# Kernel tuning notes

Hardware: AMD Instinct MI355X
Metric: run time of the kernel (lower is better)

Reference implementation:

```python
import jax, jax.numpy as jnp
import numpy as np

D_MODEL = 256
NHEAD = 8
HEAD_DIM = D_MODEL // NHEAD
LN_EPS = 1e-5


def _layernorm(x, g, b):
    mu = jnp.mean(x, axis=-1, keepdims=True)
    var = jnp.mean(jnp.square(x - mu), axis=-1, keepdims=True)
    return (x - mu) * jax.lax.rsqrt(var + LN_EPS) * g + b


def setup_inputs() -> dict:
    key = jax.random.key(0)
    ks = jax.random.split(key, 12)
    N, L, S, K = 2, 4800, 4800, 64
    x = jax.random.normal(ks[0], (N, L, D_MODEL), dtype=jnp.float32)
    source = jax.random.normal(ks[1], (N, S, D_MODEL), dtype=jnp.float32)
    # precomputed epipolar-band key indices per query ([N, L, K])
    epipolar_idx = jax.random.randint(ks[2], (N, L, K), 0, S, dtype=jnp.int32)
    w = lambda k, shape: (jax.random.normal(k, shape, dtype=jnp.float32) * 0.02)
    return {
        "x": x, "source": source, "epipolar_idx": epipolar_idx,
        "Wq": w(ks[3], (D_MODEL, D_MODEL)),
        "Wk": w(ks[4], (D_MODEL, D_MODEL)),
        "Wv": w(ks[5], (D_MODEL, D_MODEL)),
        "Wm": w(ks[6], (D_MODEL, D_MODEL)),
        "W1": w(ks[7], (2 * D_MODEL, 2 * D_MODEL)),
        "W2": w(ks[8], (2 * D_MODEL, D_MODEL)),
        "g1": jnp.ones((D_MODEL,), jnp.float32),
        "b1": jnp.zeros((D_MODEL,), jnp.float32),
        "g2": jnp.ones((D_MODEL,), jnp.float32),
        "b2": jnp.zeros((D_MODEL,), jnp.float32),
    }


def reference(x, source, epipolar_idx, Wq, Wk, Wv, Wm, W1, W2, g1, b1, g2, b2):
    N, L, _ = x.shape
    q = (x @ Wq).reshape(N, L, NHEAD, HEAD_DIM)            # [N,L,H,D]
    k = (source @ Wk).reshape(N, -1, NHEAD, HEAD_DIM)      # [N,S,H,D]
    v = (source @ Wv).reshape(N, -1, NHEAD, HEAD_DIM)
    # one-to-many gather: each query attends only to its epipolar-band keys
    gather = jax.vmap(lambda t, i: t[i])                   # [N,L,K,H,D]
    kg = gather(k, epipolar_idx)
    vg = gather(v, epipolar_idx)
    scale = 1.0 / jnp.sqrt(jnp.asarray(HEAD_DIM, x.dtype))
    scores = jnp.einsum('nlhd,nlkhd->nlhk', q, kg) * scale
    attn = jax.nn.softmax(scores, axis=-1)
    msg = jnp.einsum('nlhk,nlkhd->nlhd', attn, vg).reshape(N, L, D_MODEL)
    msg = _layernorm(msg @ Wm, g1, b1)
    h = jnp.concatenate([x, msg], axis=-1) @ W1            # [N,L,2C]
    h = jax.nn.relu(h) @ W2                                # [N,L,C]
    return x + _layernorm(h, g2, b2)
```

## Files before the change

kernel.cpp:

```cpp
#include <hip/hip_runtime.h>
#include <hip/hip_bf16.h>

#define D_MODEL 256
#define LQ 4800
#define NB 2
#define MROWS (NB * LQ)
#define LN_EPS 1e-5f

typedef unsigned int u32;
typedef unsigned short u16;
typedef __attribute__((ext_vector_type(8))) short bf16x8;
typedef __attribute__((ext_vector_type(4))) float f32x4;
typedef __attribute__((ext_vector_type(2))) _Float16 f16x2;

__device__ __forceinline__ u16 f2bf(float f) {
    __hip_bfloat16 h = __float2bfloat16(f);
    return *reinterpret_cast<u16*>(&h);
}

__device__ __forceinline__ float dot2f16(u32 a, u32 b, float c) {
#if __has_builtin(__builtin_amdgcn_fdot2)
    return __builtin_amdgcn_fdot2(__builtin_bit_cast(f16x2, a),
                                  __builtin_bit_cast(f16x2, b), c, false);
#else
    f16x2 av = __builtin_bit_cast(f16x2, a), bv = __builtin_bit_cast(f16x2, b);
    c = fmaf((float)av.x, (float)bv.x, c);
    return fmaf((float)av.y, (float)bv.y, c);
#endif
}
__device__ __forceinline__ u32 pk_fma16(u32 a, u32 b, u32 c) {
    u32 d;
    asm("v_pk_fma_f16 %0, %1, %2, %3" : "=v"(d) : "v"(a), "v"(b), "v"(c));
    return d;
}
__device__ __forceinline__ u32 pk_add16(u32 a, u32 b) {
    u32 d;
    asm("v_pk_add_f16 %0, %1, %2" : "=v"(d) : "v"(a), "v"(b));
    return d;
}
__device__ __forceinline__ u32 pkrtz(float a, float b) {
    return __builtin_bit_cast(u32, __builtin_amdgcn_cvt_pkrtz(a, b));
}
__device__ __forceinline__ void gload_lds(const u16* src, u16* dst) {
    __builtin_amdgcn_global_load_lds(
        (const __attribute__((address_space(1))) u32*)src,
        (__attribute__((address_space(3))) u32*)dst, 16, 0, 0);
}

__global__ __launch_bounds__(256) void prep_kernel(
    const float* __restrict__ x, const float* __restrict__ source,
    const float* __restrict__ Wq, const float* __restrict__ Wk,
    const float* __restrict__ Wv, const float* __restrict__ Wm,
    const float* __restrict__ W1, const float* __restrict__ W2,
    u16* __restrict__ xb, u16* __restrict__ sb,
    u16* __restrict__ Wqkvt, u16* __restrict__ Wmt,
    u16* __restrict__ W1t, u16* __restrict__ W2t)
{
    __shared__ float tile[16][17];
    const int t = threadIdx.x;
    int bid = blockIdx.x;

    if (bid < 4800) {
        const float* src = bid < 2400 ? x : source;
        u16* dst = bid < 2400 ? xb : sb;
        int b = bid < 2400 ? bid : bid - 2400;
        int i = (b * 256 + t) * 4;
        float4 v = *reinterpret_cast<const float4*>(src + i);
        ushort4 o; o.x = f2bf(v.x); o.y = f2bf(v.y); o.z = f2bf(v.z); o.w = f2bf(v.w);
        *reinterpret_cast<ushort4*>(dst + i) = o;
        return;
    }
    int sub = bid - 4800;
    const float* W; u16* Wt; int Nd, ldt, rowoff;
    if      (sub < 256)  { W = Wq; Wt = Wqkvt; Nd = 256; ldt = 256; rowoff = 0;   }
    else if (sub < 512)  { W = Wk; Wt = Wqkvt; Nd = 256; ldt = 256; rowoff = 256; sub -= 256; }
    else if (sub < 768)  { W = Wv; Wt = Wqkvt; Nd = 256; ldt = 256; rowoff = 512; sub -= 512; }
    else if (sub < 1024) { W = Wm; Wt = Wmt;   Nd = 256; ldt = 256; rowoff = 0;   sub -= 768; }
    else if (sub < 2048) { W = W1; Wt = W1t;   Nd = 512; ldt = 512; rowoff = 0;   sub -= 1024; }
    else                 { W = W2; Wt = W2t;   Nd = 256; ldt = 512; rowoff = 0;   sub -= 2048; }
    int ntiles = Nd >> 4;
    int tn = sub % ntiles, tk = sub / ntiles;
    int tx = t & 15, ty = t >> 4;
    tile[ty][tx] = W[(size_t)(tk * 16 + ty) * Nd + tn * 16 + tx];
    __syncthreads();
    Wt[(size_t)(rowoff + tn * 16 + ty) * ldt + tk * 16 + tx] = f2bf(tile[tx][ty]);
}

template<int BM, int BN>
__global__ __launch_bounds__(256) void gemm_mfma_kernel(
    const u16* __restrict__ A0, int lda0,
    const u16* __restrict__ A1, int lda1, int splitK, int nsel,
    const u16* __restrict__ Bt, int ldb,
    void* __restrict__ Cout,
    int M, int N, int K, int flags)
{
    __shared__ __align__(16) u16 As[BM * 32];
    __shared__ __align__(16) u16 Bs[BN * 32];

    constexpr int WM = BM / 2, WN = BN / 2;
    constexpr int FI = WM / 16, FJ = WN / 16;

    const int t  = threadIdx.x;
    const int l  = t & 63;
    const int w  = t >> 6;
    const int m0 = blockIdx.y * BM;
    const int n0 = blockIdx.x * BN;
    const int wr = w >> 1, wc = w & 1;

    if (nsel && n0 >= nsel) { A0 = A1; lda0 = lda1; }

    const int srow = l >> 2;
    const int sch  = (l & 3) ^ (srow & 3);

    f32x4 acc[FI][FJ];
#pragma unroll
    for (int i = 0; i < FI; ++i)
#pragma unroll
        for (int j = 0; j < FJ; ++j) acc[i][j] = (f32x4){0.f, 0.f, 0.f, 0.f};

    for (int k0 = 0; k0 < K; k0 += 32) {
        const u16* Ap; int kk, lda;
        if (splitK && k0 >= splitK) { Ap = A1; kk = k0 - splitK; lda = lda1; }
        else                        { Ap = A0; kk = k0;          lda = lda0; }

        if (BM >= 64) {
#pragma unroll
            for (int g = 0; g < BM / 64; ++g) {
                int grp = w * (BM / 64) + g;
                int row = grp * 16 + srow;
                gload_lds(Ap + (size_t)(m0 + row) * lda + kk + sch * 8, As + grp * 512);
            }
        } else if (w < BM / 16) {
            int row = w * 16 + srow;
            gload_lds(Ap + (size_t)(m0 + row) * lda + kk + sch * 8, As + w * 512);
        }
#pragma unroll
        for (int g = 0; g < BN / 64; ++g) {
            int grp = w * (BN / 64) + g;
            int row = grp * 16 + srow;
            gload_lds(Bt + (size_t)(n0 + row) * ldb + k0 + sch * 8, Bs + grp * 512);
        }
        __syncthreads();

        const int r  = l & 15;
        const int ch = l >> 4;
        bf16x8 af[FI], bfr[FJ];
#pragma unroll
        for (int i = 0; i < FI; ++i) {
            int ar = wr * WM + i * 16 + r;
            af[i] = *(const bf16x8*)((const char*)As + ar * 64 + ((ch ^ (r & 3)) * 16));
        }
#pragma unroll
        for (int j = 0; j < FJ; ++j) {
            int br = wc * WN + j * 16 + r;
            bfr[j] = *(const bf16x8*)((const char*)Bs + br * 64 + ((ch ^ (r & 3)) * 16));
        }
#pragma unroll
        for (int i = 0; i < FI; ++i)
#pragma unroll
            for (int j = 0; j < FJ; ++j)
                acc[i][j] = __builtin_amdgcn_mfma_f32_16x16x32_bf16(af[i], bfr[j], acc[i][j], 0, 0, 0);
        __syncthreads();
    }

    const int r  = l & 15;
    const int q4 = l >> 4;
#pragma unroll
    for (int i = 0; i < FI; ++i)
#pragma unroll
        for (int j = 0; j < FJ; ++j) {
            int col = n0 + wc * WN + j * 16 + r;
#pragma unroll
            for (int reg = 0; reg < 4; ++reg) {
                int row = m0 + wr * WM + i * 16 + q4 * 4 + reg;
                float vv = acc[i][j][reg];
                if (flags & 1) vv = fmaxf(vv, 0.f);
                size_t off;
                int colw, Nw;
                if (flags & 4) { off = (size_t)(col >> 8) * M * 256; colw = col & 255; Nw = 256; }
                else           { off = 0; colw = col; Nw = N; }
                if (flags & 8) {
                    _Float16 hv = (_Float16)vv;
                    ((u16*)Cout)[off + (size_t)row * Nw + colw] = __builtin_bit_cast(u16, hv);
                } else if (flags & 2) {
                    ((u16*)Cout)[off + (size_t)row * Nw + colw] = f2bf(vv);
                } else {
                    ((float*)Cout)[off + (size_t)row * Nw + colw] = vv;
                }
            }
        }
}

template<int BM, bool RESID, bool OUT_BF16>
__global__ __launch_bounds__(256) void gemm_ln_kernel(
    const u16* __restrict__ A, int lda,
    const u16* __restrict__ Bt, int ldb,
    const float* __restrict__ g, const float* __restrict__ b,
    const float* __restrict__ xres,
    void* __restrict__ Cout, int K)
{
    constexpr int WAVES_M = BM / 16;
    constexpr int WAVES_N = 4 / WAVES_M;
    constexpr int WN = 256 / WAVES_N;
    constexpr int FJ = WN / 16;

    __shared__ __align__(16) u16 As[BM * 32];
    __shared__ __align__(16) u16 Bs[256 * 32];
    __shared__ float2 red[BM][WAVES_N];

    const int t  = threadIdx.x;
    const int l  = t & 63;
    const int w  = t >> 6;
    const int m0 = blockIdx.x * BM;
    const int wr = w / WAVES_N, wc = w % WAVES_N;

    const int srow = l >> 2;
    const int sch  = (l & 3) ^ (srow & 3);

    f32x4 acc[FJ];
#pragma unroll
    for (int j = 0; j < FJ; ++j) acc[j] = (f32x4){0.f, 0.f, 0.f, 0.f};

    for (int k0 = 0; k0 < K; k0 += 32) {
        if (w < WAVES_M) {
            int row = w * 16 + srow;
            gload_lds(A + (size_t)(m0 + row) * lda + k0 + sch * 8, As + w * 512);
        }
#pragma unroll
        for (int gg = 0; gg < 4; ++gg) {
            int grp = w * 4 + gg;
            int row = grp * 16 + srow;
            gload_lds(Bt + (size_t)row * ldb + k0 + sch * 8, Bs + grp * 512);
        }
        __syncthreads();

        const int r  = l & 15;
        const int ch = l >> 4;
        bf16x8 af = *(const bf16x8*)((const char*)As + (wr * 16 + r) * 64 + ((ch ^ (r & 3)) * 16));
#pragma unroll
        for (int j = 0; j < FJ; ++j) {
            int br = wc * WN + j * 16 + r;
            bf16x8 bf = *(const bf16x8*)((const char*)Bs + br * 64 + ((ch ^ (r & 3)) * 16));
            acc[j] = __builtin_amdgcn_mfma_f32_16x16x32_bf16(af, bf, acc[j], 0, 0, 0);
        }
        __syncthreads();
    }

    const int r  = l & 15;
    const int q4 = l >> 4;

    float rs[4], rq[4];
#pragma unroll
    for (int reg = 0; reg < 4; ++reg) {
        float s = 0.f, sq = 0.f;
#pragma unroll
        for (int j = 0; j < FJ; ++j) { float vv = acc[j][reg]; s += vv; sq += vv * vv; }
        rs[reg] = s; rq[reg] = sq;
    }
#pragma unroll
    for (int off = 1; off <= 8; off <<= 1)
#pragma unroll
        for (int reg = 0; reg < 4; ++reg) {
            rs[reg] += __shfl_xor(rs[reg], off);
            rq[reg] += __shfl_xor(rq[reg], off);
        }
    if (r == 0)
#pragma unroll
        for (int reg = 0; reg < 4; ++reg)
            red[wr * 16 + q4 * 4 + reg][wc] = make_float2(rs[reg], rq[reg]);
    __syncthreads();

    float gj[FJ], bj[FJ];
#pragma unroll
    for (int j = 0; j < FJ; ++j) {
        int col = wc * WN + j * 16 + r;
        gj[j] = g[col]; bj[j] = b[col];
    }

#pragma unroll
    for (int reg = 0; reg < 4; ++reg) {
        int row = wr * 16 + q4 * 4 + reg;
        float sum = 0.f, sq = 0.f;
#pragma unroll
        for (int u = 0; u < WAVES_N; ++u) { sum += red[row][u].x; sq += red[row][u].y; }
        float mu  = sum * 0.00390625f;
        float var = sq * 0.00390625f - mu * mu;
        float rstd = rsqrtf(var + LN_EPS);
#pragma unroll
        for (int j = 0; j < FJ; ++j) {
            int col = wc * WN + j * 16 + r;
            float vv = (acc[j][reg] - mu) * rstd * gj[j] + bj[j];
            size_t oidx = (size_t)(m0 + row) * 256 + col;
            if (RESID) vv += xres[oidx];
            if (OUT_BF16) ((u16*)Cout)[oidx] = f2bf(vv);
            else          ((float*)Cout)[oidx] = vv;
        }
    }
}

__global__ __launch_bounds__(256, 8) void attn_kernel(
    const u16* __restrict__ q, const u16* __restrict__ k,
    const u16* __restrict__ v, const int* __restrict__ idx,
    u16* __restrict__ msg)
{
    const int t  = threadIdx.x;
    const int l  = t & 63;
    const int hp = t >> 6;
    const int qi = blockIdx.x;
    const int n  = qi / LQ;
    const size_t srcbase = (size_t)n * LQ * 256;

    const int o = l >> 3;
    const int c = l & 7;

    const int* idxp = idx + (size_t)qi * 64;
    int rows[8];
#pragma unroll
    for (int i = 0; i < 8; ++i) rows[i] = idxp[i * 8 + o];

    const size_t hoff = (size_t)hp * 64 + c * 8;

    uint4 kd[8];
#pragma unroll
    for (int i = 0; i < 8; ++i)
        kd[i] = *(const uint4*)(k + srcbase + (size_t)rows[i] * 256 + hoff);
    uint4 qc = *(const uint4*)(q + (size_t)qi * 256 + hoff);

    float s[8];
#pragma unroll
    for (int i = 0; i < 8; ++i) {
        float si = 0.f;
        si = dot2f16(kd[i].x, qc.x, si);
        si = dot2f16(kd[i].y, qc.y, si);
        si = dot2f16(kd[i].z, qc.z, si);
        si = dot2f16(kd[i].w, qc.w, si);
        si += __shfl_xor(si, 1);
        si += __shfl_xor(si, 2);
        s[i] = si * 0.17677669529663687f;
    }

    uint4 vd[8];
#pragma unroll
    for (int i = 0; i < 8; ++i)
        vd[i] = *(const uint4*)(v + srcbase + (size_t)rows[i] * 256 + hoff);

    float mx = s[0];
#pragma unroll
    for (int i = 1; i < 8; ++i) mx = fmaxf(mx, s[i]);
    mx = fmaxf(mx, __shfl_xor(mx, 8));
    mx = fmaxf(mx, __shfl_xor(mx, 16));
    mx = fmaxf(mx, __shfl_xor(mx, 32));
    float p[8], sum = 0.f;
#pragma unroll
    for (int i = 0; i < 8; ++i) { p[i] = __expf(s[i] - mx); sum += p[i]; }
    sum += __shfl_xor(sum, 8);
    sum += __shfl_xor(sum, 16);
    sum += __shfl_xor(sum, 32);
    float inv = 1.f / sum;

    u32 A0 = 0, A1 = 0, A2 = 0, A3 = 0;
#pragma unroll
    for (int i = 0; i < 8; ++i) {
        float pi = p[i] * inv;
        u32 pp = pkrtz(pi, pi);
        A0 = pk_fma16(pp, vd[i].x, A0);
        A1 = pk_fma16(pp, vd[i].y, A1);
        A2 = pk_fma16(pp, vd[i].z, A2);
        A3 = pk_fma16(pp, vd[i].w, A3);
    }

    const bool ob0 = (o & 1) != 0;
    const bool ob1 = (o & 2) != 0;
    {
        u32 t0 = ob0 ? A0 : A2;
        u32 t1 = ob0 ? A1 : A3;
        t0 = __shfl_xor((int)t0, 8);
        t1 = __shfl_xor((int)t1, 8);
        A0 = pk_add16(ob0 ? A2 : A0, t0);
        A1 = pk_add16(ob0 ? A3 : A1, t1);
    }
    {
        u32 u0 = ob1 ? A0 : A1;
        u0 = __shfl_xor((int)u0, 16);
        A0 = pk_add16(ob1 ? A1 : A0, u0);
    }
    A0 = pk_add16(A0, (u32)__shfl_xor((int)A0, 32));

    if (o < 4) {
        int j = 2 * (o & 1) + ((o >> 1) & 1);
        f16x2 hv = __builtin_bit_cast(f16x2, A0);
        u32 packed = (u32)f2bf((float)hv.x) | ((u32)f2bf((float)hv.y) << 16);
        *(u32*)(msg + (size_t)qi * 256 + hp * 64 + c * 8 + j * 2) = packed;
    }
}

extern "C" void kernel_launch(void* const* d_in, const int* in_sizes, int n_in,
                              void* d_out, int out_size, void* d_ws, size_t ws_size,
                              hipStream_t stream)
{
    const float* x      = (const float*)d_in[0];
    const float* source = (const float*)d_in[1];
    const int*   eidx   = (const int*)d_in[2];
    const float* Wq     = (const float*)d_in[3];
    const float* Wk     = (const float*)d_in[4];
    const float* Wv     = (const float*)d_in[5];
    const float* Wm     = (const float*)d_in[6];
    const float* W1     = (const float*)d_in[7];
    const float* W2     = (const float*)d_in[8];
    const float* g1     = (const float*)d_in[9];
    const float* b1     = (const float*)d_in[10];
    const float* g2     = (const float*)d_in[11];
    const float* b2     = (const float*)d_in[12];
    float* out = (float*)d_out;

    char* ws = (char*)d_ws;
    const size_t SZB = (size_t)MROWS * 256 * 2;
    u16* xb     = (u16*)(ws);
    u16* sb     = (u16*)(ws + SZB);
    u16* qb     = (u16*)(ws + 2 * SZB);
    u16* kb     = (u16*)(ws + 3 * SZB);
    u16* vb     = (u16*)(ws + 4 * SZB);
    u16* msgb   = (u16*)(ws + 5 * SZB);
    u16* msglnb = (u16*)(ws + 6 * SZB);
    u16* h1b    = (u16*)(ws + 7 * SZB);
    u16* Wqkvt  = (u16*)(ws + 9 * SZB);
    u16* Wmt    = Wqkvt + 768 * 256;
    u16* W1t    = Wmt + 256 * 256;
    u16* W2t    = W1t + 512 * 512;

    dim3 blk(256);

    prep_kernel<<<dim3(7360), blk, 0, stream>>>(x, source, Wq, Wk, Wv, Wm, W1, W2,
                                                xb, sb, Wqkvt, Wmt, W1t, W2t);

    gemm_mfma_kernel<64, 128><<<dim3(6, 150), blk, 0, stream>>>(
        xb, 256, sb, 256, 0, 256, Wqkvt, 256, qb, MROWS, 768, 256, 8 | 4);

    attn_kernel<<<dim3(MROWS), blk, 0, stream>>>(qb, kb, vb, eidx, msgb);

    gemm_ln_kernel<16, false, true><<<dim3(600), blk, 0, stream>>>(
        msgb, 256, Wmt, 256, g1, b1, nullptr, msglnb, 256);

    gemm_mfma_kernel<64, 128><<<dim3(4, 150), blk, 0, stream>>>(
        xb, 256, msglnb, 256, 256, 0, W1t, 512, h1b, MROWS, 512, 512, 1 | 2);

    gemm_ln_kernel<16, true, false><<<dim3(600), blk, 0, stream>>>(
        h1b, 512, W2t, 512, g2, b2, x, out, 512);
}
```

Baseline: 101.9 us.

## Fuse fp32 input conversion into QKV GEMM and fuse Wm+LN+W1 kernels

Drops the separate fp32-to-bf16 conversion of x and source. The QKV GEMM now loads fp32 tiles directly into LDS and packs them to fp16 in registers, and it also computes the x-half of the W1 product in the same launch. A new kernel chains the Wm projection, LayerNorm and the msg-half of W1 through LDS, then adds the precomputed x-half and applies ReLU, which removes the msgln round trip and one launch. Attention blocks are also remapped to interleave query positions, and the final LN GEMM switches to 32-row tiles. In exchange, the W1 x-half is rounded to bf16 before the add, and the 300-block fused kernel gives lower occupancy with heavier LDS use.

```diff
diff --git a/kernel.cpp b/kernel.cpp
--- a/kernel.cpp
+++ b/kernel.cpp
@@ -11,11 +11,16 @@
 typedef unsigned short u16;
 typedef __attribute__((ext_vector_type(8))) short bf16x8;
 typedef __attribute__((ext_vector_type(4))) float f32x4;
+typedef __attribute__((ext_vector_type(4))) u32 u32x4;
 typedef __attribute__((ext_vector_type(2))) _Float16 f16x2;
+typedef __attribute__((ext_vector_type(8))) _Float16 f16x8;
 
 __device__ __forceinline__ u16 f2bf(float f) {
     __hip_bfloat16 h = __float2bfloat16(f);
     return *reinterpret_cast<u16*>(&h);
+}
+__device__ __forceinline__ float bf2f(u32 bits16) {
+    return __uint_as_float(bits16 << 16);
 }
 
 __device__ __forceinline__ float dot2f16(u32 a, u32 b, float c) {
@@ -46,149 +51,257 @@
         (const __attribute__((address_space(1))) u32*)src,
         (__attribute__((address_space(3))) u32*)dst, 16, 0, 0);
 }
+__device__ __forceinline__ void gload_lds_f32(const float* src, u32* dst) {
+    __builtin_amdgcn_global_load_lds(
+        (const __attribute__((address_space(1))) u32*)src,
+        (__attribute__((address_space(3))) u32*)dst, 16, 0, 0);
+}
 
 __global__ __launch_bounds__(256) void prep_kernel(
-    const float* __restrict__ x, const float* __restrict__ source,
     const float* __restrict__ Wq, const float* __restrict__ Wk,
     const float* __restrict__ Wv, const float* __restrict__ Wm,
     const float* __restrict__ W1, const float* __restrict__ W2,
-    u16* __restrict__ xb, u16* __restrict__ sb,
-    u16* __restrict__ Wqkvt, u16* __restrict__ Wmt,
-    u16* __restrict__ W1t, u16* __restrict__ W2t)
+    u16* __restrict__ Wqkvh, u16* __restrict__ Wmt,
+    u16* __restrict__ W1bt, u16* __restrict__ W2t)
 {
     __shared__ float tile[16][17];
-    const int t = threadIdx.x;
-    int bid = blockIdx.x;
-
-    if (bid < 4800) {
-        const float* src = bid < 2400 ? x : source;
-        u16* dst = bid < 2400 ? xb : sb;
-        int b = bid < 2400 ? bid : bid - 2400;
-        int i = (b * 256 + t) * 4;
-        float4 v = *reinterpret_cast<const float4*>(src + i);
-        ushort4 o; o.x = f2bf(v.x); o.y = f2bf(v.y); o.z = f2bf(v.z); o.w = f2bf(v.w);
-        *reinterpret_cast<ushort4*>(dst + i) = o;
-        return;
-    }
-    int sub = bid - 4800;
-    const float* W; u16* Wt; int Nd, ldt, rowoff;
-    if      (sub < 256)  { W = Wq; Wt = Wqkvt; Nd = 256; ldt = 256; rowoff = 0;   }
-    else if (sub < 512)  { W = Wk; Wt = Wqkvt; Nd = 256; ldt = 256; rowoff = 256; sub -= 256; }
-    else if (sub < 768)  { W = Wv; Wt = Wqkvt; Nd = 256; ldt = 256; rowoff = 512; sub -= 512; }
-    else if (sub < 1024) { W = Wm; Wt = Wmt;   Nd = 256; ldt = 256; rowoff = 0;   sub -= 768; }
-    else if (sub < 2048) { W = W1; Wt = W1t;   Nd = 512; ldt = 512; rowoff = 0;   sub -= 1024; }
-    else                 { W = W2; Wt = W2t;   Nd = 256; ldt = 512; rowoff = 0;   sub -= 2048; }
-    int ntiles = Nd >> 4;
-    int tn = sub % ntiles, tk = sub / ntiles;
-    int tx = t & 15, ty = t >> 4;
+    const int t = threadIdx.x, tx = t & 15, ty = t >> 4;
+    int sub = blockIdx.x;
+
+    const float* W; int Nd, tn, tk, drow, dcol, ldt; u16* dst; bool f16o = false;
+    if (sub < 768) {
+        W = sub < 256 ? Wq : (sub < 512 ? Wk : Wv);
+        int s = sub & 255; Nd = 256; tn = s % 16; tk = s / 16;
+        dst = Wqkvh; drow = (sub >> 8) * 256 + tn * 16; dcol = tk * 16; ldt = 256; f16o = true;
+    } else if (sub < 1024) {
+        W = Wm; int s = sub - 768; Nd = 256; tn = s % 16; tk = s / 16;
+        dst = Wmt; drow = tn * 16; dcol = tk * 16; ldt = 256;
+    } else if (sub < 2048) {
+        W = W1; int s = sub - 1024; Nd = 512; tn = s % 32; tk = s / 32;
+        if (tk < 16) { dst = Wqkvh; drow = 768 + tn * 16; dcol = tk * 16; ldt = 256; f16o = true; }
+        else         { dst = W1bt;  drow = tn * 16; dcol = (tk - 16) * 16; ldt = 256; }
+    } else {
+        W = W2; int s = sub - 2048; Nd = 256; tn = s % 16; tk = s / 16;
+        dst = W2t; drow = tn * 16; dcol = tk * 16; ldt = 512;
+    }
     tile[ty][tx] = W[(size_t)(tk * 16 + ty) * Nd + tn * 16 + tx];
     __syncthreads();
-    Wt[(size_t)(rowoff + tn * 16 + ty) * ldt + tk * 16 + tx] = f2bf(tile[tx][ty]);
-}
-
-template<int BM, int BN>
-__global__ __launch_bounds__(256) void gemm_mfma_kernel(
-    const u16* __restrict__ A0, int lda0,
-    const u16* __restrict__ A1, int lda1, int splitK, int nsel,
-    const u16* __restrict__ Bt, int ldb,
-    void* __restrict__ Cout,
-    int M, int N, int K, int flags)
+    float v = tile[tx][ty];
+    u16 o;
+    if (f16o) { _Float16 h = (_Float16)v; o = __builtin_bit_cast(u16, h); }
+    else      o = f2bf(v);
+    dst[(size_t)(drow + ty) * ldt + dcol + tx] = o;
+}
+
+__global__ __launch_bounds__(256) void qkvh_kernel(
+    const float* __restrict__ x, const float* __restrict__ source,
+    const u16* __restrict__ Wqkvh,
+    u16* __restrict__ qkvb, u16* __restrict__ hx)
 {
-    __shared__ __align__(16) u16 As[BM * 32];
-    __shared__ __align__(16) u16 Bs[BN * 32];
-
-    constexpr int WM = BM / 2, WN = BN / 2;
-    constexpr int FI = WM / 16, FJ = WN / 16;
-
-    const int t  = threadIdx.x;
-    const int l  = t & 63;
-    const int w  = t >> 6;
-    const int m0 = blockIdx.y * BM;
-    const int n0 = blockIdx.x * BN;
+    __shared__ __align__(16) float As32[64 * 32];
+    __shared__ __align__(16) u16 Bs[128 * 32];
+
+    const int t = threadIdx.x, l = t & 63, w = t >> 6;
+    const int m0 = blockIdx.y * 64, n0 = blockIdx.x * 128;
     const int wr = w >> 1, wc = w & 1;
-
-    if (nsel && n0 >= nsel) { A0 = A1; lda0 = lda1; }
-
-    const int srow = l >> 2;
-    const int sch  = (l & 3) ^ (srow & 3);
-
-    f32x4 acc[FI][FJ];
-#pragma unroll
-    for (int i = 0; i < FI; ++i)
-#pragma unroll
-        for (int j = 0; j < FJ; ++j) acc[i][j] = (f32x4){0.f, 0.f, 0.f, 0.f};
-
-    for (int k0 = 0; k0 < K; k0 += 32) {
-        const u16* Ap; int kk, lda;
-        if (splitK && k0 >= splitK) { Ap = A1; kk = k0 - splitK; lda = lda1; }
-        else                        { Ap = A0; kk = k0;          lda = lda0; }
-
-        if (BM >= 64) {
-#pragma unroll
-            for (int g = 0; g < BM / 64; ++g) {
-                int grp = w * (BM / 64) + g;
-                int row = grp * 16 + srow;
-                gload_lds(Ap + (size_t)(m0 + row) * lda + kk + sch * 8, As + grp * 512);
-            }
-        } else if (w < BM / 16) {
-            int row = w * 16 + srow;
-            gload_lds(Ap + (size_t)(m0 + row) * lda + kk + sch * 8, As + w * 512);
-        }
-#pragma unroll
-        for (int g = 0; g < BN / 64; ++g) {
-            int grp = w * (BN / 64) + g;
-            int row = grp * 16 + srow;
-            gload_lds(Bt + (size_t)(n0 + row) * ldb + k0 + sch * 8, Bs + grp * 512);
+    const float* Ap = (n0 < 256 || n0 >= 768) ? x : source;
+
+    const int srow = l >> 2, sch = (l & 3) ^ (srow & 3);
+    const int arow8 = l >> 3, acw = (l & 7) ^ (arow8 & 7);
+    const int r = l & 15, ch = l >> 4;
+
+    f32x4 acc[2][4];
+#pragma unroll
+    for (int i = 0; i < 2; ++i)
+#pragma unroll
+        for (int j = 0; j < 4; ++j) acc[i][j] = (f32x4){0.f, 0.f, 0.f, 0.f};
+
+    for (int k0 = 0; k0 < 256; k0 += 32) {
+#pragma unroll
+        for (int h = 0; h < 2; ++h) {
+            const float* asrc = Ap + (size_t)(m0 + w * 16 + h * 8 + arow8) * 256 + k0 + acw * 4;
+            u32* adst = (u32*)As32 + w * 512 + h * 256;
+            gload_lds_f32(asrc, adst);
+        }
+#pragma unroll
+        for (int g = 0; g < 2; ++g) {
+            int grp = w * 2 + g;
+            gload_lds(Wqkvh + (size_t)(n0 + grp * 16 + srow) * 256 + k0 + sch * 8,
+                      Bs + grp * 512);
         }
         __syncthreads();
 
-        const int r  = l & 15;
-        const int ch = l >> 4;
-        bf16x8 af[FI], bfr[FJ];
-#pragma unroll
-        for (int i = 0; i < FI; ++i) {
-            int ar = wr * WM + i * 16 + r;
-            af[i] = *(const bf16x8*)((const char*)As + ar * 64 + ((ch ^ (r & 3)) * 16));
-        }
-#pragma unroll
-        for (int j = 0; j < FJ; ++j) {
-            int br = wc * WN + j * 16 + r;
-            bfr[j] = *(const bf16x8*)((const char*)Bs + br * 64 + ((ch ^ (r & 3)) * 16));
-        }
-#pragma unroll
-        for (int i = 0; i < FI; ++i)
-#pragma unroll
-            for (int j = 0; j < FJ; ++j)
-                acc[i][j] = __builtin_amdgcn_mfma_f32_16x16x32_bf16(af[i], bfr[j], acc[i][j], 0, 0, 0);
+        f16x8 af[2];
+#pragma unroll
+        for (int i = 0; i < 2; ++i) {
+            int ar = wr * 32 + i * 16 + r;
+            int s0 = (2 * ch) ^ (ar & 7), s1 = (2 * ch + 1) ^ (ar & 7);
+            f32x4 alo = *(const f32x4*)((const char*)As32 + ar * 128 + s0 * 16);
+            f32x4 ahi = *(const f32x4*)((const char*)As32 + ar * 128 + s1 * 16);
+            u32x4 pk = { pkrtz(alo.x, alo.y), pkrtz(alo.z, alo.w),
+                         pkrtz(ahi.x, ahi.y), pkrtz(ahi.z, ahi.w) };
+            af[i] = __builtin_bit_cast(f16x8, pk);
+        }
+#pragma unroll
+        for (int j = 0; j < 4; ++j) {
+            int br = wc * 64 + j * 16 + r;
+            f16x8 bf = *(const f16x8*)((const char*)Bs + br * 64 + ((ch ^ (r & 3)) * 16));
+#pragma unroll
+            for (int i = 0; i < 2; ++i)
+                acc[i][j] = __builtin_amdgcn_mfma_f32_16x16x32_f16(af[i], bf, acc[i][j], 0, 0, 0);
+        }
         __syncthreads();
     }
 
-    const int r  = l & 15;
     const int q4 = l >> 4;
 #pragma unroll
-    for (int i = 0; i < FI; ++i)
-#pragma unroll
-        for (int j = 0; j < FJ; ++j) {
-            int col = n0 + wc * WN + j * 16 + r;
+    for (int i = 0; i < 2; ++i)
+#pragma unroll
+        for (int j = 0; j < 4; ++j) {
+            int col = n0 + wc * 64 + j * 16 + r;
 #pragma unroll
             for (int reg = 0; reg < 4; ++reg) {
-                int row = m0 + wr * WM + i * 16 + q4 * 4 + reg;
+                int row = m0 + wr * 32 + i * 16 + q4 * 4 + reg;
                 float vv = acc[i][j][reg];
-                if (flags & 1) vv = fmaxf(vv, 0.f);
-                size_t off;
-                int colw, Nw;
-                if (flags & 4) { off = (size_t)(col >> 8) * M * 256; colw = col & 255; Nw = 256; }
-                else           { off = 0; colw = col; Nw = N; }
-                if (flags & 8) {
+                if (col < 768) {
                     _Float16 hv = (_Float16)vv;
-                    ((u16*)Cout)[off + (size_t)row * Nw + colw] = __builtin_bit_cast(u16, hv);
-                } else if (flags & 2) {
-                    ((u16*)Cout)[off + (size_t)row * Nw + colw] = f2bf(vv);
+                    qkvb[(size_t)(col >> 8) * MROWS * 256 + (size_t)row * 256 + (col & 255)] =
+                        __builtin_bit_cast(u16, hv);
                 } else {
-                    ((float*)Cout)[off + (size_t)row * Nw + colw] = vv;
+                    hx[(size_t)row * 512 + (col - 768)] = f2bf(vv);
                 }
             }
         }
+}
+
+__global__ __launch_bounds__(256) void wm_w1_kernel(
+    const u16* __restrict__ msg, const u16* __restrict__ Wmt,
+    const u16* __restrict__ W1bt, const u16* __restrict__ hx,
+    const float* __restrict__ g1, const float* __restrict__ b1,
+    u16* __restrict__ h1b)
+{
+    __shared__ __align__(16) u16 As[32 * 32];
+    __shared__ __align__(16) u16 Bs[512 * 32];
+    __shared__ __align__(16) u16 mln[32 * 256];
+    __shared__ float2 red[32][2];
+
+    const int t = threadIdx.x, l = t & 63, w = t >> 6;
+    const int m0 = blockIdx.x * 32;
+    const int srow = l >> 2, sch = (l & 3) ^ (srow & 3);
+    const int r = l & 15, ch = l >> 4, q4 = l >> 4;
+
+    {
+        const int wr = w >> 1, wc = w & 1;
+        f32x4 acc[8];
+#pragma unroll
+        for (int j = 0; j < 8; ++j) acc[j] = (f32x4){0.f, 0.f, 0.f, 0.f};
+
+        for (int k0 = 0; k0 < 256; k0 += 32) {
+            if (w < 2)
+                gload_lds(msg + (size_t)(m0 + w * 16 + srow) * 256 + k0 + sch * 8, As + w * 512);
+#pragma unroll
+            for (int g = 0; g < 4; ++g) {
+                int grp = w * 4 + g;
+                gload_lds(Wmt + (size_t)(grp * 16 + srow) * 256 + k0 + sch * 8, Bs + grp * 512);
+            }
+            __syncthreads();
+            bf16x8 af = *(const bf16x8*)((const char*)As + (wr * 16 + r) * 64 + ((ch ^ (r & 3)) * 16));
+#pragma unroll
+            for (int j = 0; j < 8; ++j) {
+                int br = wc * 128 + j * 16 + r;
+                bf16x8 bf = *(const bf16x8*)((const char*)Bs + br * 64 + ((ch ^ (r & 3)) * 16));
+                acc[j] = __builtin_amdgcn_mfma_f32_16x16x32_bf16(af, bf, acc[j], 0, 0, 0);
+            }
+            __syncthreads();
+        }
+
+        float rs[4], rq[4];
+#pragma unroll
+        for (int reg = 0; reg < 4; ++reg) {
+            float s = 0.f, sq = 0.f;
+#pragma unroll
+            for (int j = 0; j < 8; ++j) { float vv = acc[j][reg]; s += vv; sq += vv * vv; }
+            rs[reg] = s; rq[reg] = sq;
+        }
+#pragma unroll
+        for (int off = 1; off <= 8; off <<= 1)
+#pragma unroll
+            for (int reg = 0; reg < 4; ++reg) {
+                rs[reg] += __shfl_xor(rs[reg], off);
+                rq[reg] += __shfl_xor(rq[reg], off);
+            }
+        if (r == 0)
+#pragma unroll
+            for (int reg = 0; reg < 4; ++reg)
+                red[wr * 16 + q4 * 4 + reg][wc] = make_float2(rs[reg], rq[reg]);
+        __syncthreads();
+
+#pragma unroll
+        for (int reg = 0; reg < 4; ++reg) {
+            int row = wr * 16 + q4 * 4 + reg;
+            float sum = red[row][0].x + red[row][1].x;
+            float sq  = red[row][0].y + red[row][1].y;
+            float mu  = sum * 0.00390625f;
+            float var = sq * 0.00390625f - mu * mu;
+            float rstd = rsqrtf(var + LN_EPS);
+#pragma unroll
+            for (int j = 0; j < 8; ++j) {
+                int col = wc * 128 + j * 16 + r;
+                float vv = (acc[j][reg] - mu) * rstd * g1[col] + b1[col];
+                int cc = col >> 3, slot = cc ^ (row & 7);
+                *(u16*)((char*)mln + row * 512 + slot * 16 + (col & 7) * 2) = f2bf(vv);
+            }
+        }
+        __syncthreads();
+    }
+
+    {
+        f32x4 acc2[2][8];
+#pragma unroll
+        for (int i = 0; i < 2; ++i)
+#pragma unroll
+            for (int j = 0; j < 8; ++j) acc2[i][j] = (f32x4){0.f, 0.f, 0.f, 0.f};
+
+        for (int k0 = 0; k0 < 256; k0 += 32) {
+#pragma unroll
+            for (int g = 0; g < 8; ++g) {
+                int row = w * 128 + g * 16 + srow;
+                gload_lds(W1bt + (size_t)row * 256 + k0 + sch * 8, Bs + (w * 8 + g) * 512);
+            }
+            __syncthreads();
+            bf16x8 af2[2];
+#pragma unroll
+            for (int i = 0; i < 2; ++i) {
+                int ar = i * 16 + r;
+                int c0 = (k0 >> 3) + ch;
+                af2[i] = *(const bf16x8*)((const char*)mln + ar * 512 + ((c0 ^ (ar & 7)) * 16));
+            }
+#pragma unroll
+            for (int j = 0; j < 8; ++j) {
+                int br = w * 128 + j * 16 + r;
+                bf16x8 bf = *(const bf16x8*)((const char*)Bs + br * 64 + ((ch ^ (r & 3)) * 16));
+#pragma unroll
+                for (int i = 0; i < 2; ++i)
+                    acc2[i][j] = __builtin_amdgcn_mfma_f32_16x16x32_bf16(af2[i], bf, acc2[i][j], 0, 0, 0);
+            }
+            __syncthreads();
+        }
+
+#pragma unroll
+        for (int i = 0; i < 2; ++i)
+#pragma unroll
+            for (int j = 0; j < 8; ++j) {
+                int col = w * 128 + j * 16 + r;
+#pragma unroll
+                for (int reg = 0; reg < 4; ++reg) {
+                    int row = i * 16 + q4 * 4 + reg;
+                    size_t oidx = (size_t)(m0 + row) * 512 + col;
+                    float vv = acc2[i][j][reg] + bf2f((u32)hx[oidx]);
+                    vv = fmaxf(vv, 0.f);
+                    h1b[oidx] = f2bf(vv);
+                }
+            }
+    }
 }
 
 template<int BM, bool RESID, bool OUT_BF16>
@@ -306,7 +419,9 @@
     const int t  = threadIdx.x;
     const int l  = t & 63;
     const int hp = t >> 6;
-    const int qi = blockIdx.x;
+    const int bid = blockIdx.x;
+    const int x8 = bid & 7, jj = bid >> 3;
+    const int qi = (x8 < 4) ? (x8 * 1200 + jj) : (LQ + (x8 - 4) * 1200 + jj);
     const int n  = qi / LQ;
     const size_t srcbase = (size_t)n * LQ * 256;
 
@@ -415,35 +530,28 @@
 
     char* ws = (char*)d_ws;
     const size_t SZB = (size_t)MROWS * 256 * 2;
-    u16* xb     = (u16*)(ws);
-    u16* sb     = (u16*)(ws + SZB);
-    u16* qb     = (u16*)(ws + 2 * SZB);
-    u16* kb     = (u16*)(ws + 3 * SZB);
-    u16* vb     = (u16*)(ws + 4 * SZB);
-    u16* msgb   = (u16*)(ws + 5 * SZB);
-    u16* msglnb = (u16*)(ws + 6 * SZB);
-    u16* h1b    = (u16*)(ws + 7 * SZB);
-    u16* Wqkvt  = (u16*)(ws + 9 * SZB);
-    u16* Wmt    = Wqkvt + 768 * 256;
-    u16* W1t    = Wmt + 256 * 256;
-    u16* W2t    = W1t + 512 * 512;
+    u16* qb     = (u16*)(ws);
+    u16* kb     = (u16*)(ws + SZB);
+    u16* vb     = (u16*)(ws + 2 * SZB);
+    u16* msgb   = (u16*)(ws + 3 * SZB);
+    u16* hx     = (u16*)(ws + 4 * SZB);
+    u16* h1b    = (u16*)(ws + 6 * SZB);
+    u16* Wqkvh  = (u16*)(ws + 8 * SZB);
+    u16* Wmt    = Wqkvh + 1280 * 256;
+    u16* W1bt   = Wmt + 256 * 256;
+    u16* W2t    = W1bt + 512 * 256;
 
     dim3 blk(256);
 
-    prep_kernel<<<dim3(7360), blk, 0, stream>>>(x, source, Wq, Wk, Wv, Wm, W1, W2,
-                                                xb, sb, Wqkvt, Wmt, W1t, W2t);
-
-    gemm_mfma_kernel<64, 128><<<dim3(6, 150), blk, 0, stream>>>(
-        xb, 256, sb, 256, 0, 256, Wqkvt, 256, qb, MROWS, 768, 256, 8 | 4);
+    prep_kernel<<<dim3(2560), blk, 0, stream>>>(Wq, Wk, Wv, Wm, W1, W2,
+                                                Wqkvh, Wmt, W1bt, W2t);
+
+    qkvh_kernel<<<dim3(10, 150), blk, 0, stream>>>(x, source, Wqkvh, qb, hx);
 
     attn_kernel<<<dim3(MROWS), blk, 0, stream>>>(qb, kb, vb, eidx, msgb);
 
-    gemm_ln_kernel<16, false, true><<<dim3(600), blk, 0, stream>>>(
-        msgb, 256, Wmt, 256, g1, b1, nullptr, msglnb, 256);
-
-    gemm_mfma_kernel<64, 128><<<dim3(4, 150), blk, 0, stream>>>(
-        xb, 256, msglnb, 256, 256, 0, W1t, 512, h1b, MROWS, 512, 512, 1 | 2);
-
-    gemm_ln_kernel<16, true, false><<<dim3(600), blk, 0, stream>>>(
+    wm_w1_kernel<<<dim3(300), blk, 0, stream>>>(msgb, Wmt, W1bt, hx, g1, b1, h1b);
+
+    gemm_ln_kernel<32, true, false><<<dim3(300), blk, 0, stream>>>(
         h1b, 512, W2t, 512, g2, b2, x, out, 512);
 }
```

After: 97.76 us. -4.1%, faster.
